# Performance work log

Hardware: AMD Instinct MI355X
Metric: run time of the kernel (lower is better)

Reference implementation:

```python
import jax, jax.numpy as jnp
import numpy as np

B, IN, H, OUT = 128, 256, 128, 32

def setup_inputs() -> dict:
    key = jax.random.key(0)
    ks = jax.random.split(key, 7)
    return {
        "input": jax.random.normal(ks[0], (B, IN), dtype=jnp.float32),
        "sigma_psi": jax.random.normal(ks[1], (1, IN, H, OUT), dtype=jnp.float32),
        "chi": jax.random.normal(ks[2], (1, IN, H, 1), dtype=jnp.float32),
        "sigma_eps": jax.random.normal(ks[3], (1, H, OUT), dtype=jnp.float32),
        "eta": jax.random.normal(ks[4], (1, H, OUT), dtype=jnp.float32),
        "mu_phi": jax.random.normal(ks[5], (1, OUT), dtype=jnp.float32),
        "sigma_phi": jax.random.normal(ks[6], (1, OUT), dtype=jnp.float32),
    }

def reference(input, sigma_psi, chi, sigma_eps, eta, mu_phi, sigma_phi):
    # x: (B, IN, 1, 1); broadcast diff against chi (1, IN, H, 1)
    x = input.reshape(-1, input.shape[1], 1, 1)
    # s: (B, H, OUT) = sum over in_features of (sigma_psi*(chi-x))^2
    s = jnp.sum((sigma_psi * (chi - x)) ** 2, axis=1)
    w = 1.0 / (s + sigma_eps ** 2)                       # (B, H, OUT)
    denom = 1.0 + sigma_phi ** 2 * jnp.sum(w, axis=1)    # (B, OUT)
    post_mu = (mu_phi + sigma_phi ** 2 * jnp.sum(w * eta, axis=1)) / denom
    post_sigma2 = sigma_phi ** 2 / denom
    return post_mu, post_sigma2
```

## Files before the change

kernel.cpp:

```cpp
#include <hip/hip_runtime.h>
#include <hip/hip_bf16.h>

#define B_   128
#define IN_  256
#define H_   128
#define OUT_ 32
#define BT   8
#define HT   8

__global__ __launch_bounds__(256) void o1u_main(
    const float* __restrict__ input,
    const float* __restrict__ sigma_psi,
    const float* __restrict__ chi,
    const float* __restrict__ sigma_eps,
    const float* __restrict__ eta,
    float* __restrict__ sum_w,
    float* __restrict__ sum_weta)
{
    const int tid = threadIdx.x;
    const int o  = tid & 31;
    const int hl = tid >> 5;
    const int h_base = blockIdx.x * HT;
    const int b_base = blockIdx.y * BT;
    const int h = h_base + hl;

    __shared__ float x_s[BT][IN_];
    __shared__ float chi_s[HT][IN_ + 1];

    for (int idx = tid; idx < BT * IN_; idx += 256) {
        int b = idx >> 8;
        int i = idx & (IN_ - 1);
        x_s[b][i] = input[(b_base + b) * IN_ + i];
    }
    for (int idx = tid; idx < HT * IN_; idx += 256) {
        int hh = idx >> 8;
        int i  = idx & (IN_ - 1);
        chi_s[hh][i] = chi[i * H_ + (h_base + hh)];
    }
    __syncthreads();

    float s[BT];
#pragma unroll
    for (int b = 0; b < BT; ++b) s[b] = 0.0f;

    const float* sp_ptr = sigma_psi + (size_t)h * OUT_ + o;
#pragma unroll 4
    for (int i = 0; i < IN_; ++i) {
        float sp = sp_ptr[(size_t)i * (H_ * OUT_)];
        float c  = chi_s[hl][i];
#pragma unroll
        for (int b = 0; b < BT; ++b) {
            float d = sp * (c - x_s[b][i]);
            s[b] = fmaf(d, d, s[b]);
        }
    }

    const float se = sigma_eps[h * OUT_ + o];
    const float et = eta[h * OUT_ + o];
    const float se2 = se * se;

    __shared__ float red_w[HT][BT][OUT_];
    __shared__ float red_we[HT][BT][OUT_];
#pragma unroll
    for (int b = 0; b < BT; ++b) {
        float w = 1.0f / (s[b] + se2);
        red_w[hl][b][o]  = w;
        red_we[hl][b][o] = w * et;
    }
    __syncthreads();

    const int rb = tid >> 5;
    const int ro = tid & 31;
    float sw = 0.0f, swe = 0.0f;
#pragma unroll
    for (int k = 0; k < HT; ++k) {
        sw  += red_w[k][rb][ro];
        swe += red_we[k][rb][ro];
    }
    atomicAdd(&sum_w[(b_base + rb) * OUT_ + ro], sw);
    atomicAdd(&sum_weta[(b_base + rb) * OUT_ + ro], swe);
}

__global__ __launch_bounds__(256) void o1u_final(
    const float* __restrict__ sum_w,
    const float* __restrict__ sum_weta,
    const float* __restrict__ mu_phi,
    const float* __restrict__ sigma_phi,
    float* __restrict__ out)
{
    const int idx = blockIdx.x * 256 + threadIdx.x;
    if (idx >= B_ * OUT_) return;
    const int o = idx & (OUT_ - 1);
    float sp = sigma_phi[o];
    float sp2 = sp * sp;
    float denom = 1.0f + sp2 * sum_w[idx];
    float inv = 1.0f / denom;
    out[idx] = (mu_phi[o] + sp2 * sum_weta[idx]) * inv;
    out[B_ * OUT_ + idx] = sp2 * inv;
}

extern "C" void kernel_launch(void* const* d_in, const int* in_sizes, int n_in,
                              void* d_out, int out_size, void* d_ws, size_t ws_size,
                              hipStream_t stream) {
    const float* input     = (const float*)d_in[0];
    const float* sigma_psi = (const float*)d_in[1];
    const float* chi       = (const float*)d_in[2];
    const float* sigma_eps = (const float*)d_in[3];
    const float* eta       = (const float*)d_in[4];
    const float* mu_phi    = (const float*)d_in[5];
    const float* sigma_phi = (const float*)d_in[6];
    float* out = (float*)d_out;
    float* ws  = (float*)d_ws;

    float* sum_w    = ws;
    float* sum_weta = ws + B_ * OUT_;

    hipMemsetAsync(d_ws, 0, 2 * B_ * OUT_ * sizeof(float), stream);

    dim3 grid(H_ / HT, B_ / BT);
    o1u_main<<<grid, 256, 0, stream>>>(input, sigma_psi, chi, sigma_eps, eta,
                                       sum_w, sum_weta);
    o1u_final<<<(B_ * OUT_ + 255) / 256, 256, 0, stream>>>(sum_w, sum_weta,
                                                           mu_phi, sigma_phi, out);
}
```

Baseline: 93.48 us.

## Factor squared sigma_psi out, precompute squared diffs, split IN across warps, drop atomics

The squared difference (chi - x)^2 is computed once per block and stored in shared memory, and the sum over IN becomes sp^2 * diff^2, so the inner loop is a single FMA per element. Each thread covers 4 outputs via float4 loads of sigma_psi, and the IN dimension is split across eight warp groups that are reduced afterward in shared memory. The memset and global atomics are replaced by per-H-block partial buffers that the final kernel sums, which needs more workspace and adds a reduction pass. More blocks with HT=4 and launch bounds of 2 blocks per unit aim for better occupancy.

```diff
diff --git a/kernel.cpp b/kernel.cpp
--- a/kernel.cpp
+++ b/kernel.cpp
@@ -1,71 +1,79 @@
 #include <hip/hip_runtime.h>
-#include <hip/hip_bf16.h>
 
 #define B_   128
 #define IN_  256
 #define H_   128
 #define OUT_ 32
+#define HT   4
 #define BT   8
-#define HT   8
+#define NHB  (H_ / HT)
+#define NBB  (B_ / BT)
+#define DIFF_STRIDE 2056
+#define SM_FLOATS   (HT * DIFF_STRIDE)
 
-__global__ __launch_bounds__(256) void o1u_main(
+__global__ __launch_bounds__(256, 2) void o1u_main(
     const float* __restrict__ input,
     const float* __restrict__ sigma_psi,
     const float* __restrict__ chi,
     const float* __restrict__ sigma_eps,
     const float* __restrict__ eta,
-    float* __restrict__ sum_w,
-    float* __restrict__ sum_weta)
+    float* __restrict__ sw_part,
+    float* __restrict__ swe_part)
 {
     const int tid = threadIdx.x;
-    const int o  = tid & 31;
-    const int hl = tid >> 5;
-    const int h_base = blockIdx.x * HT;
+    const int ig = tid >> 5;
+    const int hl = (tid >> 3) & 3;
+    const int og = tid & 7;
+    const int hb = blockIdx.x;
+    const int h_base = hb * HT;
     const int b_base = blockIdx.y * BT;
-    const int h = h_base + hl;
 
-    __shared__ float x_s[BT][IN_];
-    __shared__ float chi_s[HT][IN_ + 1];
+    __shared__ __align__(16) float sm[SM_FLOATS];
 
-    for (int idx = tid; idx < BT * IN_; idx += 256) {
-        int b = idx >> 8;
-        int i = idx & (IN_ - 1);
-        x_s[b][i] = input[(b_base + b) * IN_ + i];
-    }
-    for (int idx = tid; idx < HT * IN_; idx += 256) {
-        int hh = idx >> 8;
-        int i  = idx & (IN_ - 1);
-        chi_s[hh][i] = chi[i * H_ + (h_base + hh)];
+#pragma unroll
+    for (int k = 0; k < (HT * IN_ * BT) / 256; ++k) {
+        int flat = k * 256 + tid;
+        int b  = flat & 7;
+        int i  = (flat >> 3) & 255;
+        int hh = flat >> 11;
+        float e = chi[i * H_ + (h_base + hh)] - input[(b_base + b) * IN_ + i];
+        sm[hh * DIFF_STRIDE + (flat & 2047)] = e * e;
     }
     __syncthreads();
 
-    float s[BT];
+    const float* sp_base = sigma_psi + (size_t)(h_base + hl) * OUT_ + og * 4;
+    const float* drow = sm + hl * DIFF_STRIDE;
+    float s[BT][4];
 #pragma unroll
-    for (int b = 0; b < BT; ++b) s[b] = 0.0f;
+    for (int b = 0; b < BT; ++b)
+#pragma unroll
+        for (int j = 0; j < 4; ++j) s[b][j] = 0.0f;
 
-    const float* sp_ptr = sigma_psi + (size_t)h * OUT_ + o;
 #pragma unroll 4
-    for (int i = 0; i < IN_; ++i) {
-        float sp = sp_ptr[(size_t)i * (H_ * OUT_)];
-        float c  = chi_s[hl][i];
+    for (int k = 0; k < IN_ / 8; ++k) {
+        int i = ig * 32 + k;
+        float4 sp = *(const float4*)(sp_base + (size_t)i * (H_ * OUT_));
+        float4 sp2;
+        sp2.x = sp.x * sp.x; sp2.y = sp.y * sp.y;
+        sp2.z = sp.z * sp.z; sp2.w = sp.w * sp.w;
+        const float4* dp = (const float4*)(drow + i * 8);
+        float4 eA = dp[0];
+        float4 eB = dp[1];
+        float ev[8] = {eA.x, eA.y, eA.z, eA.w, eB.x, eB.y, eB.z, eB.w};
 #pragma unroll
         for (int b = 0; b < BT; ++b) {
-            float d = sp * (c - x_s[b][i]);
-            s[b] = fmaf(d, d, s[b]);
+            s[b][0] = fmaf(sp2.x, ev[b], s[b][0]);
+            s[b][1] = fmaf(sp2.y, ev[b], s[b][1]);
+            s[b][2] = fmaf(sp2.z, ev[b], s[b][2]);
+            s[b][3] = fmaf(sp2.w, ev[b], s[b][3]);
         }
     }
 
-    const float se = sigma_eps[h * OUT_ + o];
-    const float et = eta[h * OUT_ + o];
-    const float se2 = se * se;
-
-    __shared__ float red_w[HT][BT][OUT_];
-    __shared__ float red_we[HT][BT][OUT_];
+    __syncthreads();
 #pragma unroll
     for (int b = 0; b < BT; ++b) {
-        float w = 1.0f / (s[b] + se2);
-        red_w[hl][b][o]  = w;
-        red_we[hl][b][o] = w * et;
+        float4 v; v.x = s[b][0]; v.y = s[b][1]; v.z = s[b][2]; v.w = s[b][3];
+        *(float4*)(sm + ig * 1024 + hl * 256 + b * 32 + og * 4) = v;
     }
     __syncthreads();
 
@@ -73,29 +81,39 @@
     const int ro = tid & 31;
     float sw = 0.0f, swe = 0.0f;
 #pragma unroll
-    for (int k = 0; k < HT; ++k) {
-        sw  += red_w[k][rb][ro];
-        swe += red_we[k][rb][ro];
+    for (int hh = 0; hh < HT; ++hh) {
+        float sfull = 0.0f;
+#pragma unroll
+        for (int g = 0; g < 8; ++g)
+            sfull += sm[g * 1024 + hh * 256 + rb * 32 + ro];
+        float se = sigma_eps[(h_base + hh) * OUT_ + ro];
+        float w = 1.0f / fmaf(se, se, sfull);
+        sw += w;
+        swe += w * eta[(h_base + hh) * OUT_ + ro];
     }
-    atomicAdd(&sum_w[(b_base + rb) * OUT_ + ro], sw);
-    atomicAdd(&sum_weta[(b_base + rb) * OUT_ + ro], swe);
+    sw_part[((size_t)hb * B_ + (b_base + rb)) * OUT_ + ro] = sw;
+    swe_part[((size_t)hb * B_ + (b_base + rb)) * OUT_ + ro] = swe;
 }
 
-__global__ __launch_bounds__(256) void o1u_final(
-    const float* __restrict__ sum_w,
-    const float* __restrict__ sum_weta,
+__global__ __launch_bounds__(64) void o1u_final(
+    const float* __restrict__ sw_part,
+    const float* __restrict__ swe_part,
     const float* __restrict__ mu_phi,
     const float* __restrict__ sigma_phi,
     float* __restrict__ out)
 {
-    const int idx = blockIdx.x * 256 + threadIdx.x;
-    if (idx >= B_ * OUT_) return;
+    const int idx = blockIdx.x * 64 + threadIdx.x;
     const int o = idx & (OUT_ - 1);
+    float sw = 0.0f, swe = 0.0f;
+#pragma unroll 8
+    for (int hb = 0; hb < NHB; ++hb) {
+        sw  += sw_part[hb * (B_ * OUT_) + idx];
+        swe += swe_part[hb * (B_ * OUT_) + idx];
+    }
     float sp = sigma_phi[o];
     float sp2 = sp * sp;
-    float denom = 1.0f + sp2 * sum_w[idx];
-    float inv = 1.0f / denom;
-    out[idx] = (mu_phi[o] + sp2 * sum_weta[idx]) * inv;
+    float inv = 1.0f / fmaf(sp2, sw, 1.0f);
+    out[idx] = fmaf(sp2, swe, mu_phi[o]) * inv;
     out[B_ * OUT_ + idx] = sp2 * inv;
 }
 
@@ -112,14 +130,12 @@
     float* out = (float*)d_out;
     float* ws  = (float*)d_ws;
 
-    float* sum_w    = ws;
-    float* sum_weta = ws + B_ * OUT_;
+    float* sw_part  = ws;
+    float* swe_part = ws + NHB * B_ * OUT_;
 
-    hipMemsetAsync(d_ws, 0, 2 * B_ * OUT_ * sizeof(float), stream);
-
-    dim3 grid(H_ / HT, B_ / BT);
+    dim3 grid(NHB, NBB);
     o1u_main<<<grid, 256, 0, stream>>>(input, sigma_psi, chi, sigma_eps, eta,
-                                       sum_w, sum_weta);
-    o1u_final<<<(B_ * OUT_ + 255) / 256, 256, 0, stream>>>(sum_w, sum_weta,
-                                                           mu_phi, sigma_phi, out);
+                                       sw_part, swe_part);
+    o1u_final<<<(B_ * OUT_) / 64, 64, 0, stream>>>(sw_part, swe_part,
+                                                   mu_phi, sigma_phi, out);
 }
```

Result: faster. 80.26 us (-14.1%).
